# Performance work log

Hardware: AMD Instinct MI355X
Metric: run time of the kernel (lower is better)

## Reference

```python
import jax, jax.numpy as jnp
import numpy as np

B, N, K = 2, 1024, 16
D_MODEL, D_ELLIP, N_HEADS = 768, 128, 8
NF = D_MODEL // 6            # sinusoidal freqs per coordinate
MAX_LOG_FREQ = 7.0
ENC_H = max(1, N_HEADS // 2) # ellipsoid encoder heads
ENC_FF = 2048                # torch TransformerEncoderLayer default dim_feedforward


def setup_inputs() -> dict:
    key = jax.random.key(0)
    ks = jax.random.split(key, 20)
    rn = lambda k, sh, sc=1.0: jax.random.normal(k, sh, dtype=jnp.float32) * sc
    w = lambda k, o, i: rn(k, (o, i), 1.0 / np.sqrt(i))
    inp = {}
    inp['s'] = rn(ks[0], (B, N, D_MODEL))
    inp['R'] = rn(ks[1], (B, N, 3, 3))
    inp['t'] = rn(ks[2], (B, N, 3))
    inp['ellip_tokens'] = rn(ks[3], (B, K, D_ELLIP))
    inp['mu'] = rn(ks[4], (B, K, 3))
    inp['Sigma'] = rn(ks[5], (B, K, 3, 3))
    inp['ellip_mask'] = jnp.ones((B, K), dtype=jnp.bool_)
    # main attention params (torch Linear convention: [out, in])
    inp['mix_w'] = w(ks[6], 6 * NF, 6 * NF)
    inp['lin_cov_w'] = w(ks[7], D_MODEL, 9)
    inp['q_w'] = w(ks[8], D_MODEL, D_MODEL)
    inp['k_w'] = w(ks[9], D_MODEL, 2 * D_MODEL)
    inp['v_w'] = w(ks[10], D_MODEL, D_MODEL + D_ELLIP)
    inp['o_w'] = w(ks[11], D_MODEL, D_MODEL)
    # ellipsoid TransformerEncoderLayer params (post-norm, eval mode)
    inp['enc_in_w'] = w(ks[12], 3 * D_ELLIP, D_ELLIP)
    inp['enc_in_b'] = jnp.zeros((3 * D_ELLIP,), jnp.float32)
    inp['enc_out_w'] = w(ks[13], D_ELLIP, D_ELLIP)
    inp['enc_out_b'] = jnp.zeros((D_ELLIP,), jnp.float32)
    inp['lin1_w'] = w(ks[14], ENC_FF, D_ELLIP)
    inp['lin1_b'] = jnp.zeros((ENC_FF,), jnp.float32)
    inp['lin2_w'] = w(ks[15], D_ELLIP, ENC_FF)
    inp['lin2_b'] = jnp.zeros((D_ELLIP,), jnp.float32)
    inp['ln1_g'] = jnp.ones((D_ELLIP,), jnp.float32)
    inp['ln1_b'] = jnp.zeros((D_ELLIP,), jnp.float32)
    inp['ln2_g'] = jnp.ones((D_ELLIP,), jnp.float32)
    inp['ln2_b'] = jnp.zeros((D_ELLIP,), jnp.float32)
    return inp


def _layernorm(x, g, b, eps=1e-5):
    m = x.mean(-1, keepdims=True)
    v = ((x - m) ** 2).mean(-1, keepdims=True)
    return (x - m) / jnp.sqrt(v + eps) * g + b


def _fwd(s, R, t, ellip_tokens, mu, Sigma, mix_w, lin_cov_w, q_w, k_w, v_w, o_w,
         enc_in_w, enc_in_b, enc_out_w, enc_out_b, lin1_w, lin1_b, lin2_w, lin2_b,
         ln1_g, ln1_b, ln2_g, ln2_b, ellip_mask):
    # --- ellipsoid self-attn encoder (single post-norm layer, eval mode) ---
    x = ellip_tokens                                   # [B,K,de]
    qkv = x @ enc_in_w.T + enc_in_b
    q, kk, v = jnp.split(qkv, 3, axis=-1)
    dhe = D_ELLIP // ENC_H
    qh = q.reshape(B, K, ENC_H, dhe)
    kh = kk.reshape(B, K, ENC_H, dhe)
    vh = v.reshape(B, K, ENC_H, dhe)
    sc = jnp.einsum('bqhd,bkhd->bhqk', qh, kh) / np.sqrt(dhe).astype(np.float32)
    ao = jnp.einsum('bhqk,bkhd->bqhd', jax.nn.softmax(sc, -1), vh).reshape(B, K, D_ELLIP)
    ao = ao @ enc_out_w.T + enc_out_b
    x = _layernorm(x + ao, ln1_g, ln1_b)
    ff = jax.nn.relu(x @ lin1_w.T + lin1_b) @ lin2_w.T + lin2_b
    e = _layernorm(x + ff, ln2_g, ln2_b)               # [B,K,de]
    # --- per-query local frame transforms ---
    diff = mu[:, None, :, :] - t[:, :, None, :]        # [B,N,K,3]
    r = jnp.einsum('bnji,bnkj->bnki', R, diff)         # R^T @ diff
    C = jnp.einsum('bnji,bkjl,bnlm->bnkim', R, Sigma, R)  # R^T Sigma R [B,N,K,3,3]
    # --- sinusoidal posenc (sin first, then cos; flatten coord-major) ---
    freqs = 2.0 ** jnp.linspace(0.0, MAX_LOG_FREQ, NF).astype(jnp.float32)
    xf = r[..., None] * freqs                          # [B,N,K,3,NF]
    feat = jnp.concatenate([jnp.sin(xf), jnp.cos(xf)], axis=-2).reshape(B, N, K, 6 * NF)
    pos = feat @ mix_w.T                               # [B,N,K,d]
    cov = C.reshape(B, N, K, 9) @ lin_cov_w.T          # [B,N,K,d]
    K_mat = jnp.concatenate([pos, cov], -1) @ k_w.T    # [B,N,K,d]
    eB = jnp.broadcast_to(e[:, None, :, :], (B, N, K, D_ELLIP))
    V_mat = jnp.concatenate([pos, eB], -1) @ v_w.T     # [B,N,K,d]
    Q = s @ q_w.T                                      # [B,N,d]
    dh = D_MODEL // N_HEADS
    Qh = Q.reshape(B, N, N_HEADS, dh)
    Kh = K_mat.reshape(B, N, K, N_HEADS, dh)
    Vh = V_mat.reshape(B, N, K, N_HEADS, dh)
    scores = jnp.einsum('bnhd,bnkhd->bnhk', Qh, Kh) / np.sqrt(dh).astype(np.float32)
    scores = scores + (1.0 - ellip_mask.astype(scores.dtype))[:, None, None, :] * -10000.0
    attn = jax.nn.softmax(scores, -1)                  # [B,N,H,K]
    out = jnp.einsum('bnhk,bnkhd->bnhd', attn, Vh).reshape(B, N, D_MODEL)
    return out @ o_w.T


def reference(s, R, t, ellip_tokens, mu, Sigma, mix_w, lin_cov_w, q_w, k_w, v_w, o_w,
              enc_in_w, enc_in_b, enc_out_w, enc_out_b, lin1_w, lin1_b, lin2_w, lin2_b,
              ln1_g, ln1_b, ln2_g, ln2_b, ellip_mask):
    return _fwd(s, R, t, ellip_tokens, mu, Sigma, mix_w, lin_cov_w, q_w, k_w, v_w, o_w,
                enc_in_w, enc_in_b, enc_out_w, enc_out_b, lin1_w, lin1_b, lin2_w, lin2_b,
                ln1_g, ln1_b, ln2_g, ln2_b, ellip_mask)
```

## Files before the change

kernel.cpp:

```cpp
#include <hip/hip_runtime.h>
#include <math.h>

#define BB     2
#define SEQ    1024
#define KTOK   16
#define DM     768
#define DE     128
#define NH     8
#define DHD    96
#define EH     4
#define DHE    32
#define EFF    2048

typedef short short8 __attribute__((ext_vector_type(8)));
typedef float f32x4 __attribute__((ext_vector_type(4)));
typedef unsigned short ushort_t;

__device__ __forceinline__ void split2(float x, ushort_t& h, ushort_t& l) {
  unsigned u = __float_as_uint(x);
  unsigned hb = (u + 0x7fffu + ((u >> 16) & 1u)) >> 16;
  float hf = __uint_as_float(hb << 16);
  float r = x - hf;
  unsigned u2 = __float_as_uint(r);
  unsigned lb = (u2 + 0x7fffu + ((u2 >> 16) & 1u)) >> 16;
  h = (ushort_t)hb;
  l = (ushort_t)lb;
}

typedef const unsigned int __attribute__((address_space(1)))* gas_p;
typedef unsigned int __attribute__((address_space(3)))* las_p;
__device__ __forceinline__ void load_lds16(const ushort_t* g, ushort_t* l) {
  __builtin_amdgcn_global_load_lds((gas_p)g, (las_p)l, 16, 0, 0);
}

template<int OMODE, bool ADD>
__device__ __forceinline__ void gemm_body(
    ushort_t (*AhB)[2048], ushort_t (*AlB)[2048],
    ushort_t (*BhB)[2048], ushort_t (*BlB)[2048],
    const ushort_t* A, int lda, int aC0, int aLoOff,
    const ushort_t* B, int ldb, int bC0, int bLoOff,
    void* Cv, int ldc, int cLoOff,
    const float* av, int ldadd,
    int row0, int col0, int N, int K)
{
  int tid = threadIdx.x;
  int wave = tid >> 6, lane = tid & 63;
  int quad = lane >> 4, mrow = lane & 15;
  int wm = (wave >> 1) * 32, wn = (wave & 1) * 32;
  int sr = tid >> 2, q8 = (tid & 3) << 3;
  int wbase = wave << 9;
  f32x4 acc[2][2] = {};

  const ushort_t* pa = A + (long)(row0 + sr) * lda + (aC0 + q8);
  const ushort_t* pb = B + (long)(col0 + sr) * ldb + (bC0 + q8);

  load_lds16(pa, &AhB[0][wbase]);
  load_lds16(pa + aLoOff, &AlB[0][wbase]);
  load_lds16(pb, &BhB[0][wbase]);
  load_lds16(pb + bLoOff, &BlB[0][wbase]);

  int buf = 0;
  for (int k0 = 0; k0 < K; k0 += 32) {
    __syncthreads();
    if (k0 + 32 < K) {
      int kn = k0 + 32;
      load_lds16(pa + kn, &AhB[buf ^ 1][wbase]);
      load_lds16(pa + aLoOff + kn, &AlB[buf ^ 1][wbase]);
      load_lds16(pb + kn, &BhB[buf ^ 1][wbase]);
      load_lds16(pb + bLoOff + kn, &BlB[buf ^ 1][wbase]);
    }
    short8 fah[2], fal[2], fbh[2], fbl[2];
    #pragma unroll
    for (int t = 0; t < 2; t++) {
      fah[t] = *(const short8*)&AhB[buf][(wm + t * 16 + mrow) * 32 + (quad << 3)];
      fal[t] = *(const short8*)&AlB[buf][(wm + t * 16 + mrow) * 32 + (quad << 3)];
      fbh[t] = *(const short8*)&BhB[buf][(wn + t * 16 + mrow) * 32 + (quad << 3)];
      fbl[t] = *(const short8*)&BlB[buf][(wn + t * 16 + mrow) * 32 + (quad << 3)];
    }
    #pragma unroll
    for (int mt = 0; mt < 2; mt++)
      #pragma unroll
      for (int nt = 0; nt < 2; nt++) {
        f32x4 c = acc[mt][nt];
        c = __builtin_amdgcn_mfma_f32_16x16x32_bf16(fah[mt], fbh[nt], c, 0, 0, 0);
        c = __builtin_amdgcn_mfma_f32_16x16x32_bf16(fal[mt], fbh[nt], c, 0, 0, 0);
        c = __builtin_amdgcn_mfma_f32_16x16x32_bf16(fah[mt], fbl[nt], c, 0, 0, 0);
        acc[mt][nt] = c;
      }
    buf ^= 1;
  }
  float* Cf = (float*)Cv;
  ushort_t* Cs = (ushort_t*)Cv;
  #pragma unroll
  for (int mt = 0; mt < 2; mt++)
    #pragma unroll
    for (int nt = 0; nt < 2; nt++) {
      int col = col0 + wn + nt * 16 + mrow;
      if (col >= N) continue;
      int rb = row0 + wm + mt * 16 + (quad << 2);
      #pragma unroll
      for (int rr = 0; rr < 4; rr++) {
        float v = acc[mt][nt][rr];
        if (ADD) v += av[(long)(rb + rr) * ldadd + col];
        if (OMODE == 0) {
          Cf[(long)(rb + rr) * ldc + col] = v;
        } else {
          ushort_t h, l;
          split2(v, h, l);
          Cs[(long)(rb + rr) * ldc + col] = h;
          Cs[(long)(rb + rr) * ldc + cLoOff + col] = l;
        }
      }
    }
}

template<int OMODE, bool ADD>
__global__ __launch_bounds__(256) void gemm3t(
    const ushort_t* __restrict__ A, int lda, int aKstep, int aLoOff,
    const ushort_t* __restrict__ B, long bOffZ, int ldb, int bKstep, int bLoOff,
    void* __restrict__ Cv, int ldc, int cOffZ, int cLoOff,
    const float* __restrict__ addv, int ldadd, int addOffZ,
    int M, int N, int K)
{
  __shared__ ushort_t Ah[2][2048], Al[2][2048], Bh[2][2048], Bl[2][2048];
  int z = blockIdx.z;
  void* Cz = (OMODE == 0) ? (void*)((float*)Cv + (long)z * cOffZ)
                          : (void*)((ushort_t*)Cv + (long)z * cOffZ);
  gemm_body<OMODE, ADD>(Ah, Al, Bh, Bl,
      A, lda, z * aKstep, aLoOff,
      B + (long)z * bOffZ, ldb, z * bKstep, bLoOff,
      Cz, ldc, cLoOff,
      ADD ? addv + (long)z * addOffZ : nullptr, ldadd,
      blockIdx.y * 64, blockIdx.x * 64, N, K);
}

__global__ __launch_bounds__(256) void combo1(
    const float* __restrict__ s, const float* __restrict__ q_w,
    const float* __restrict__ o_w, const float* __restrict__ k_w,
    const float* __restrict__ v_w,
    ushort_t* __restrict__ sS, ushort_t* __restrict__ qwS,
    ushort_t* __restrict__ owS, ushort_t* __restrict__ kwS,
    ushort_t* __restrict__ vwS,
    const float* __restrict__ mix_w, ushort_t* __restrict__ mixTS,
    const float* __restrict__ tok, const float* __restrict__ enc_in_w,
    const float* __restrict__ enc_in_b, float* __restrict__ qkv,
    const float* __restrict__ lin_cov_w, float* __restrict__ Bk9)
{
  int r = blockIdx.x, tid = threadIdx.x;
  if (r < 3840) {
    const float* in; int ldin; ushort_t* out; int base;
    if (r < 1536)      { in = s;   ldin = DM;      out = sS;  base = 0; }
    else if (r < 2112) { in = q_w; ldin = DM;      out = qwS; base = 1536; }
    else if (r < 2688) { in = o_w; ldin = DM;      out = owS; base = 2112; }
    else if (r < 3264) { in = k_w; ldin = 2 * DM;  out = kwS; base = 2688; }
    else               { in = v_w; ldin = DM + DE; out = vwS; base = 3264; }
    long i = (long)(r - base) * 256 + tid;
    int rr = (int)(i / 192), c4 = (int)(i % 192) << 2;
    float4 v = *(const float4*)(in + (long)rr * ldin + c4);
    ushort_t h[4], l[4];
    split2(v.x, h[0], l[0]);
    split2(v.y, h[1], l[1]);
    split2(v.z, h[2], l[2]);
    split2(v.w, h[3], l[3]);
    ushort_t* orow = out + (long)rr * 1536;
    ushort4 hv; hv.x = h[0]; hv.y = h[1]; hv.z = h[2]; hv.w = h[3];
    ushort4 lv; lv.x = l[0]; lv.y = l[1]; lv.z = l[2]; lv.w = l[3];
    *(ushort4*)(orow + c4) = hv;
    *(ushort4*)(orow + DM + c4) = lv;
  } else if (r < 3984) {
    __shared__ float tile[64][65];
    int idx = r - 3840;
    int n0 = (idx % 12) * 64, k0 = (idx / 12) * 64;
    #pragma unroll
    for (int p = 0; p < 16; p++) {
      int q = p * 256 + tid;
      int rr = q >> 6, cc = q & 63;
      tile[rr][cc] = mix_w[(long)(k0 + rr) * DM + n0 + cc];
    }
    __syncthreads();
    #pragma unroll
    for (int p = 0; p < 16; p++) {
      int q = p * 256 + tid;
      int nr = q >> 6, kc = q & 63;
      ushort_t h, l;
      split2(tile[kc][nr], h, l);
      mixTS[(long)(n0 + nr) * 1536 + (k0 + kc)] = h;
      mixTS[(long)(n0 + nr) * 1536 + DM + (k0 + kc)] = l;
    }
  } else if (r < 4016) {
    __shared__ float xr[DE];
    int tkn = r - 3984;
    if (tid < DE) xr[tid] = tok[tkn * DE + tid];
    __syncthreads();
    for (int o = tid; o < 3 * DE; o += 256) {
      float acc = enc_in_b[o];
      const float4* wr = (const float4*)(enc_in_w + (long)o * DE);
      #pragma unroll 8
      for (int j = 0; j < DE / 4; j++) {
        float4 p = wr[j];
        acc = fmaf(p.x, xr[j * 4 + 0], acc);
        acc = fmaf(p.y, xr[j * 4 + 1], acc);
        acc = fmaf(p.z, xr[j * 4 + 2], acc);
        acc = fmaf(p.w, xr[j * 4 + 3], acc);
      }
      qkv[tkn * 384 + o] = acc;
    }
  } else {
    int idx = (r - 4016) * 256 + tid;
    if (idx < DM * 9) {
      int rr = idx / 9, p = idx % 9;
      const float* kr = k_w + (long)rr * (2 * DM) + DM;
      float acc = 0.f;
      for (int j = 0; j < DM; j++) acc = fmaf(kr[j], lin_cov_w[j * 9 + p], acc);
      Bk9[idx] = acc;
    }
  }
}

union MegaSmem {
  struct { ushort_t Ah[2][2048], Al[2][2048], Bh[2][2048], Bl[2][2048]; } g;
  struct {
    float qkvs[KTOK][384];
    float scl2[EH][KTOK], at2[EH][KTOK];
    float ao[DE], x1s[DE], el[DE];
    float ff1L[EFF];
    float part[256];
    float red[4], stats[2];
  } e;
};

__global__ __launch_bounds__(256) void mega1(
    const ushort_t* __restrict__ sS, const ushort_t* __restrict__ qwS,
    const ushort_t* __restrict__ mixTS, const ushort_t* __restrict__ kwS,
    const ushort_t* __restrict__ vwS,
    ushort_t* __restrict__ QS, ushort_t* __restrict__ AkTS,
    ushort_t* __restrict__ AvS,
    const float* __restrict__ tok, const float* __restrict__ qkvG,
    const float* __restrict__ out_w, const float* __restrict__ out_b,
    const float* __restrict__ ln1_g, const float* __restrict__ ln1_b,
    const float* __restrict__ lin1_w, const float* __restrict__ lin1_b,
    const float* __restrict__ lin2_w, const float* __restrict__ lin2_b,
    const float* __restrict__ ln2_g, const float* __restrict__ ln2_b,
    const float* __restrict__ v_w, float* __restrict__ evec)
{
  __shared__ MegaSmem sm;
  int blk = blockIdx.x, tid = threadIdx.x;
  if (blk < 672) {
    if (blk < 384) {
      gemm_body<1, false>(sm.g.Ah, sm.g.Al, sm.g.Bh, sm.g.Bl,
                          sS, 1536, 0, DM, qwS, 1536, 0, DM,
                          QS, 1536, DM, nullptr, 0,
                          (blk / 12) * 64, (blk % 12) * 64, DM, DM);
    } else if (blk < 528) {
      int t2 = blk - 384;
      gemm_body<1, false>(sm.g.Ah, sm.g.Al, sm.g.Bh, sm.g.Bl,
                          mixTS, 1536, 0, DM, kwS, 1536, 0, DM,
                          AkTS, 1536, DM, nullptr, 0,
                          (t2 / 12) * 64, (t2 % 12) * 64, DM, DM);
    } else {
      int t2 = blk - 528;
      gemm_body<1, false>(sm.g.Ah, sm.g.Al, sm.g.Bh, sm.g.Bl,
                          vwS, 1536, 0, DM, mixTS, 1536, 0, DM,
                          AvS, 1536, DM, nullptr, 0,
                          (t2 / 12) * 64, (t2 % 12) * 64, DM, DM);
    }
    return;
  }
  int idx = blk - 672;
  int b = idx >> 4, tk = idx & 15;
  for (int i = tid; i < KTOK * 384; i += 256)
    sm.e.qkvs[i / 384][i % 384] = qkvG[b * KTOK * 384 + i];
  __syncthreads();
  if (tid < EH * KTOK) {
    int h = tid >> 4, kk = tid & 15;
    float a = 0.f;
    #pragma unroll 8
    for (int d = 0; d < DHE; d++)
      a = fmaf(sm.e.qkvs[tk][h * DHE + d], sm.e.qkvs[kk][DE + h * DHE + d], a);
    sm.e.scl2[h][kk] = a * 0.17677669529663687f;
  }
  __syncthreads();
  if (tid < EH) {
    float m = -1e30f;
    for (int kk = 0; kk < KTOK; kk++) m = fmaxf(m, sm.e.scl2[tid][kk]);
    float smx = 0.f;
    for (int kk = 0; kk < KTOK; kk++) { float e = expf(sm.e.scl2[tid][kk] - m); sm.e.at2[tid][kk] = e; smx += e; }
    float inv = 1.f / smx;
    for (int kk = 0; kk < KTOK; kk++) sm.e.at2[tid][kk] *= inv;
  }
  __syncthreads();
  if (tid < DE) {
    int h = tid / DHE;
    float a = 0.f;
    #pragma unroll
    for (int kk = 0; kk < KTOK; kk++) a = fmaf(sm.e.at2[h][kk], sm.e.qkvs[kk][256 + tid], a);
    sm.e.ao[tid] = a;
  }
  __syncthreads();
  float val = 0.f;
  if (tid < DE) {
    float a = out_b[tid];
    const float4* wr = (const float4*)(out_w + (long)tid * DE);
    #pragma unroll 8
    for (int j = 0; j < DE / 4; j++) {
      float4 p = wr[j];
      a = fmaf(p.x, sm.e.ao[j * 4 + 0], a);
      a = fmaf(p.y, sm.e.ao[j * 4 + 1], a);
      a = fmaf(p.z, sm.e.ao[j * 4 + 2], a);
      a = fmaf(p.w, sm.e.ao[j * 4 + 3], a);
    }
    val = tok[idx * DE + tid] + a;
  }
  {
    float v = val;
    #pragma unroll
    for (int off = 32; off > 0; off >>= 1) v += __shfl_down(v, off);
    if ((tid & 63) == 0) sm.e.red[tid >> 6] = v;
    __syncthreads();
    if (tid == 0) sm.e.stats[0] = (sm.e.red[0] + sm.e.red[1] + sm.e.red[2] + sm.e.red[3]) * (1.f / DE);
    __syncthreads();
    float d = (tid < DE) ? (val - sm.e.stats[0]) : 0.f;
    float v2 = d * d;
    #pragma unroll
    for (int off = 32; off > 0; off >>= 1) v2 += __shfl_down(v2, off);
    if ((tid & 63) == 0) sm.e.red[tid >> 6] = v2;
    __syncthreads();
    if (tid == 0) sm.e.stats[1] = rsqrtf((sm.e.red[0] + sm.e.red[1] + sm.e.red[2] + sm.e.red[3]) * (1.f / DE) + 1e-5f);
    __syncthreads();
    if (tid < DE) sm.e.x1s[tid] = (val - sm.e.stats[0]) * sm.e.stats[1] * ln1_g[tid] + ln1_b[tid];
    __syncthreads();
  }
  for (int f = tid; f < EFF; f += 256) {
    float a = lin1_b[f];
    const float4* wr = (const float4*)(lin1_w + (long)f * DE);
    #pragma unroll 8
    for (int j = 0; j < DE / 4; j++) {
      float4 p = wr[j];
      a = fmaf(p.x, sm.e.x1s[j * 4 + 0], a);
      a = fmaf(p.y, sm.e.x1s[j * 4 + 1], a);
      a = fmaf(p.z, sm.e.x1s[j * 4 + 2], a);
      a = fmaf(p.w, sm.e.x1s[j * 4 + 3], a);
    }
    sm.e.ff1L[f] = fmaxf(a, 0.f);
  }
  __syncthreads();
  {
    int j = tid >> 1, half = tid & 1;
    const float4* wr = (const float4*)(lin2_w + (long)j * EFF + half * 1024);
    const float4* fr = (const float4*)(sm.e.ff1L + half * 1024);
    float a = 0.f;
    #pragma unroll 8
    for (int i = 0; i < 256; i++) {
      float4 p = wr[i], q = fr[i];
      a = fmaf(p.x, q.x, a);
      a = fmaf(p.y, q.y, a);
      a = fmaf(p.z, q.z, a);
      a = fmaf(p.w, q.w, a);
    }
    sm.e.part[tid] = a;
  }
  __syncthreads();
  float t2v = 0.f;
  if (tid < DE) t2v = sm.e.x1s[tid] + lin2_b[tid] + sm.e.part[2 * tid] + sm.e.part[2 * tid + 1];
  {
    float v = t2v;
    #pragma unroll
    for (int off = 32; off > 0; off >>= 1) v += __shfl_down(v, off);
    if ((tid & 63) == 0) sm.e.red[tid >> 6] = v;
    __syncthreads();
    if (tid == 0) sm.e.stats[0] = (sm.e.red[0] + sm.e.red[1] + sm.e.red[2] + sm.e.red[3]) * (1.f / DE);
    __syncthreads();
    float d = (tid < DE) ? (t2v - sm.e.stats[0]) : 0.f;
    float v2 = d * d;
    #pragma unroll
    for (int off = 32; off > 0; off >>= 1) v2 += __shfl_down(v2, off);
    if ((tid & 63) == 0) sm.e.red[tid >> 6] = v2;
    __syncthreads();
    if (tid == 0) sm.e.stats[1] = rsqrtf((sm.e.red[0] + sm.e.red[1] + sm.e.red[2] + sm.e.red[3]) * (1.f / DE) + 1e-5f);
    __syncthreads();
    if (tid < DE) sm.e.el[tid] = (t2v - sm.e.stats[0]) * sm.e.stats[1] * ln2_g[tid] + ln2_b[tid];
    __syncthreads();
  }
  #pragma unroll
  for (int q = 0; q < 3; q++) {
    int d = tid + (q << 8);
    float a = 0.f;
    const float4* wr = (const float4*)(v_w + (long)d * (DM + DE) + DM);
    #pragma unroll 8
    for (int j = 0; j < DE / 4; j++) {
      float4 p = wr[j];
      a = fmaf(p.x, sm.e.el[j * 4 + 0], a);
      a = fmaf(p.y, sm.e.el[j * 4 + 1], a);
      a = fmaf(p.z, sm.e.el[j * 4 + 2], a);
      a = fmaf(p.w, sm.e.el[j * 4 + 3], a);
    }
    evec[idx * DM + d] = a;
  }
}

__global__ __launch_bounds__(256) void qa_qb(
    const ushort_t* __restrict__ QS, const ushort_t* __restrict__ AkTS,
    float* __restrict__ QA, const float* __restrict__ Bk9,
    float* __restrict__ QB)
{
  __shared__ ushort_t Ah[2][2048], Al[2][2048], Bh[2][2048], Bl[2][2048];
  int r = blockIdx.x;
  if (r < 3072) {
    int z = r / 384, rr = r % 384;
    gemm_body<0, false>(Ah, Al, Bh, Bl,
        QS, 1536, z * DHD, DM, AkTS, 1536, z * DHD, DM,
        (void*)(QA + (long)z * DM), NH * DM, 0, nullptr, 0,
        (rr / 12) * 64, (rr % 12) * 64, DM, DHD);
  } else {
    int idx = (r - 3072) * 256 + threadIdx.x;
    if (idx < BB * SEQ * NH * 9) {
      int bn = idx / 72, rem = idx % 72, h = rem / 9, p = rem % 9;
      const ushort_t* qr = QS + (long)bn * 1536 + h * DHD;
      float acc = 0.f;
      for (int k = 0; k < DHD; k++) {
        float q = __uint_as_float((unsigned)qr[k] << 16) +
                  __uint_as_float((unsigned)qr[DM + k] << 16);
        acc = fmaf(q, Bk9[(h * DHD + k) * 9 + p], acc);
      }
      QB[idx] = acc;
    }
  }
}

__global__ __launch_bounds__(256) void main_attn(
    const float* __restrict__ Rg, const float* __restrict__ tg,
    const float* __restrict__ mug, const float* __restrict__ Sigg,
    const float* __restrict__ QAg, const float* __restrict__ QBg,
    const float* __restrict__ evec, ushort_t* __restrict__ wfeatS,
    float* __restrict__ outeG)
{
  int bn = blockIdx.x;
  int b = bn >> 10;
  int tid = threadIdx.x;
  int w = tid >> 6, lane = tid & 63;
  int h0 = 2 * w, h1 = 2 * w + 1;
  __shared__ float Rm[9], tm[3];
  __shared__ float rK[KTOK][3];
  __shared__ float C9[KTOK][9];
  __shared__ float featL[8][772];
  __shared__ float QBl[NH][12];
  __shared__ float scl[NH][KTOK];
  __shared__ float attnl[NH][KTOK];
  __shared__ float freqsL[128];
  float4 qa0[3], qa1[3];
  {
    const float* qbase = QAg + (long)bn * (NH * DM);
    #pragma unroll
    for (int g = 0; g < 3; g++) {
      qa0[g] = *(const float4*)&qbase[h0 * DM + g * 256 + (lane << 2)];
      qa1[g] = *(const float4*)&qbase[h1 * DM + g * 256 + (lane << 2)];
    }
  }
  if (tid < 9) Rm[tid] = Rg[bn * 9 + tid];
  if (tid >= 16 && tid < 19) tm[tid - 16] = tg[bn * 3 + (tid - 16)];
  if (tid >= 32 && tid < 32 + NH * 9) {
    int q = tid - 32;
    QBl[q / 9][q % 9] = QBg[bn * (NH * 9) + q];
  }
  if (tid >= 128) {
    const float step = 7.0f / 127.0f;
    freqsL[tid - 128] = exp2f(step * (float)(tid - 128));
  }
  __syncthreads();
  if (tid < KTOK) {
    int k = tid;
    float diff[3];
    #pragma unroll
    for (int j = 0; j < 3; j++) diff[j] = mug[(b * KTOK + k) * 3 + j] - tm[j];
    #pragma unroll
    for (int i = 0; i < 3; i++) {
      float a = 0.f;
      #pragma unroll
      for (int j = 0; j < 3; j++) a = fmaf(Rm[j * 3 + i], diff[j], a);
      rK[k][i] = a;
    }
    float SR[9];
    const float* Sg = Sigg + (b * KTOK + k) * 9;
    #pragma unroll
    for (int j = 0; j < 3; j++)
      #pragma unroll
      for (int m2 = 0; m2 < 3; m2++) {
        float a = 0.f;
        #pragma unroll
        for (int l = 0; l < 3; l++) a = fmaf(Sg[j * 3 + l], Rm[l * 3 + m2], a);
        SR[j * 3 + m2] = a;
      }
    #pragma unroll
    for (int i = 0; i < 3; i++)
      #pragma unroll
      for (int m2 = 0; m2 < 3; m2++) {
        float a = 0.f;
        #pragma unroll
        for (int j = 0; j < 3; j++) a = fmaf(Rm[j * 3 + i], SR[j * 3 + m2], a);
        C9[k][i * 3 + m2] = a;
      }
  }
  __syncthreads();
  for (int half = 0; half < 2; half++) {
    int kb = half * 8;
    for (int c = tid; c < 768; c += 256) {
      int k = c / 96, f0 = (c % 96) << 2;
      int coord = f0 >> 7;
      float rv = rK[kb + k][coord];
      float4 fr = *(const float4*)&freqsL[f0 & 127];
      float4 sv, cv;
      __sincosf(rv * fr.x, &sv.x, &cv.x);
      __sincosf(rv * fr.y, &sv.y, &cv.y);
      __sincosf(rv * fr.z, &sv.z, &cv.z);
      __sincosf(rv * fr.w, &sv.w, &cv.w);
      *(float4*)&featL[k][f0] = sv;
      *(float4*)&featL[k][384 + f0] = cv;
    }
    __syncthreads();
    for (int k = 0; k < 8; k++) {
      float a0 = 0.f, a1 = 0.f;
      #pragma unroll
      for (int g = 0; g < 3; g++) {
        float4 fv = *(const float4*)&featL[k][g * 256 + (lane << 2)];
        a0 = fmaf(qa0[g].x, fv.x, a0); a0 = fmaf(qa0[g].y, fv.y, a0);
        a0 = fmaf(qa0[g].z, fv.z, a0); a0 = fmaf(qa0[g].w, fv.w, a0);
        a1 = fmaf(qa1[g].x, fv.x, a1); a1 = fmaf(qa1[g].y, fv.y, a1);
        a1 = fmaf(qa1[g].z, fv.z, a1); a1 = fmaf(qa1[g].w, fv.w, a1);
      }
      #pragma unroll
      for (int off = 32; off > 0; off >>= 1) {
        a0 += __shfl_down(a0, off);
        a1 += __shfl_down(a1, off);
      }
      if (lane == 0) { scl[h0][kb + k] = a0; scl[h1][kb + k] = a1; }
    }
    __syncthreads();
  }
  if (tid < NH) {
    int h = tid;
    float vals[KTOK];
    float m = -1e30f;
    for (int k = 0; k < KTOK; k++) {
      float a = scl[h][k];
      #pragma unroll
      for (int p = 0; p < 9; p++) a = fmaf(C9[k][p], QBl[h][p], a);
      a *= 0.10206207261596575f;
      vals[k] = a;
      m = fmaxf(m, a);
    }
    float sm = 0.f;
    for (int k = 0; k < KTOK; k++) { float e = expf(vals[k] - m); attnl[h][k] = e; sm += e; }
    float inv = 1.f / sm;
    for (int k = 0; k < KTOK; k++) attnl[h][k] *= inv;
  }
  __syncthreads();
  float at0[KTOK], at1[KTOK];
  #pragma unroll
  for (int k = 0; k < KTOK; k++) { at0[k] = attnl[h0][k]; at1[k] = attnl[h1][k]; }
  float4 wf0[3] = {}, wf1[3] = {};
  for (int pass = 0; pass < 2; pass++) {
    int kb = (pass == 0) ? 8 : 0;
    if (pass == 1) {
      __syncthreads();
      for (int c = tid; c < 768; c += 256) {
        int k = c / 96, f0 = (c % 96) << 2;
        int coord = f0 >> 7;
        float rv = rK[k][coord];
        float4 fr = *(const float4*)&freqsL[f0 & 127];
        float4 sv, cv;
        __sincosf(rv * fr.x, &sv.x, &cv.x);
        __sincosf(rv * fr.y, &sv.y, &cv.y);
        __sincosf(rv * fr.z, &sv.z, &cv.z);
        __sincosf(rv * fr.w, &sv.w, &cv.w);
        *(float4*)&featL[k][f0] = sv;
        *(float4*)&featL[k][384 + f0] = cv;
      }
      __syncthreads();
    }
    #pragma unroll
    for (int g = 0; g < 3; g++) {
      float4 s0 = wf0[g], s1 = wf1[g];
      #pragma unroll
      for (int k = 0; k < 8; k++) {
        float4 fv = *(const float4*)&featL[k][g * 256 + (lane << 2)];
        float w0 = at0[kb + k], w1 = at1[kb + k];
        s0.x = fmaf(w0, fv.x, s0.x); s0.y = fmaf(w0, fv.y, s0.y);
        s0.z = fmaf(w0, fv.z, s0.z); s0.w = fmaf(w0, fv.w, s0.w);
        s1.x = fmaf(w1, fv.x, s1.x); s1.y = fmaf(w1, fv.y, s1.y);
        s1.z = fmaf(w1, fv.z, s1.z); s1.w = fmaf(w1, fv.w, s1.w);
      }
      wf0[g] = s0; wf1[g] = s1;
    }
  }
  {
    ushort_t* wrow = wfeatS + (long)bn * (2 * NH * DM);
    #pragma unroll
    for (int g = 0; g < 3; g++) {
      int jj = g * 256 + (lane << 2);
      ushort4 hv, lv;
      split2(wf0[g].x, hv.x, lv.x); split2(wf0[g].y, hv.y, lv.y);
      split2(wf0[g].z, hv.z, lv.z); split2(wf0[g].w, hv.w, lv.w);
      *(ushort4*)(wrow + h0 * DM + jj) = hv;
      *(ushort4*)(wrow + NH * DM + h0 * DM + jj) = lv;
      split2(wf1[g].x, hv.x, lv.x); split2(wf1[g].y, hv.y, lv.y);
      split2(wf1[g].z, hv.z, lv.z); split2(wf1[g].w, hv.w, lv.w);
      *(ushort4*)(wrow + h1 * DM + jj) = hv;
      *(ushort4*)(wrow + NH * DM + h1 * DM + jj) = lv;
    }
  }
  for (int d = tid; d < DM; d += 256) {
    int h = d / DHD;
    float acc = 0.f;
    #pragma unroll
    for (int k = 0; k < KTOK; k++)
      acc = fmaf(attnl[h][k], evec[(b * KTOK + k) * DM + d], acc);
    outeG[(long)bn * DM + d] = acc;
  }
}

extern "C" void kernel_launch(void* const* d_in, const int* in_sizes, int n_in,
                              void* d_out, int out_size, void* d_ws, size_t ws_size,
                              hipStream_t stream) {
  const float* s    = (const float*)d_in[0];
  const float* R    = (const float*)d_in[1];
  const float* t    = (const float*)d_in[2];
  const float* tok  = (const float*)d_in[3];
  const float* mu   = (const float*)d_in[4];
  const float* Sig  = (const float*)d_in[5];
  const float* mix_w     = (const float*)d_in[7];
  const float* lin_cov_w = (const float*)d_in[8];
  const float* q_w  = (const float*)d_in[9];
  const float* k_w  = (const float*)d_in[10];
  const float* v_w  = (const float*)d_in[11];
  const float* o_w  = (const float*)d_in[12];
  const float* enc_in_w  = (const float*)d_in[13];
  const float* enc_in_b  = (const float*)d_in[14];
  const float* enc_out_w = (const float*)d_in[15];
  const float* enc_out_b = (const float*)d_in[16];
  const float* lin1_w = (const float*)d_in[17];
  const float* lin1_b = (const float*)d_in[18];
  const float* lin2_w = (const float*)d_in[19];
  const float* lin2_b = (const float*)d_in[20];
  const float* ln1_g = (const float*)d_in[21];
  const float* ln1_b = (const float*)d_in[22];
  const float* ln2_g = (const float*)d_in[23];
  const float* ln2_b = (const float*)d_in[24];
  float* out = (float*)d_out;
  char* wsb  = (char*)d_ws;

  const int BN = BB * SEQ;
  float* qkv  = (float*)(wsb);
  float* evec = (float*)(wsb + 344064);
  float* Bk9  = (float*)(wsb + 442368);
  char* p = wsb + 470016;
  ushort_t* qwS   = (ushort_t*)p;  p += 2359296;
  ushort_t* owS   = (ushort_t*)p;  p += 2359296;
  ushort_t* kwS   = (ushort_t*)p;  p += 2359296;
  ushort_t* vwS   = (ushort_t*)p;  p += 2359296;
  ushort_t* mixTS = (ushort_t*)p;  p += 2359296;
  ushort_t* AkTS  = (ushort_t*)p;  p += 2359296;
  ushort_t* AvS   = (ushort_t*)p;  p += 2359296;
  ushort_t* sS    = (ushort_t*)p;  p += 6291456;
  ushort_t* QS    = (ushort_t*)p;  p += 6291456;
  float*    QB    = (float*)p;     p += 589824;
  float*    oute  = (float*)p;     p += 6291456;
  float*    QA    = (float*)p;     p += 50331648;
  ushort_t* wfeatS = (ushort_t*)QA;
  ushort_t* US     = sS;

  dim3 blk(256);

  combo1<<<4043, blk, 0, stream>>>(s, q_w, o_w, k_w, v_w,
                                   sS, qwS, owS, kwS, vwS,
                                   mix_w, mixTS,
                                   tok, enc_in_w, enc_in_b, qkv,
                                   lin_cov_w, Bk9);
  mega1<<<704, blk, 0, stream>>>(sS, qwS, mixTS, kwS, vwS, QS, AkTS, AvS,
                                 tok, qkv, enc_out_w, enc_out_b,
                                 ln1_g, ln1_b, lin1_w, lin1_b,
                                 lin2_w, lin2_b, ln2_g, ln2_b, v_w, evec);
  qa_qb<<<3648, blk, 0, stream>>>(QS, AkTS, QA, Bk9, QB);
  main_attn<<<BN, blk, 0, stream>>>(R, t, mu, Sig, QA, QB, evec, wfeatS, oute);
  gemm3t<1, true><<<dim3(2, 32, NH), blk, 0, stream>>>(
      wfeatS, 2 * NH * DM, DM, NH * DM,  AvS, (long)DHD * 1536, 1536, 0, DM,
      US, 1536, DHD, DM,  oute, DM, DHD,  BN, DHD, DM);
  gemm3t<0, false><<<dim3(12, 32, 1), blk, 0, stream>>>(
      US, 1536, 0, DM,  owS, 0, 1536, 0, DM,
      out, DM, 0, 0,  nullptr, 0, 0,  BN, DM, DM);
}
```

Measured before the change: 362.1 us.

## Split encoder FFN across blocks, defer attn·evec into GEMM epilogue, swizzle LDS

The per-token encoder FFN used to run serially in 32 tail blocks of mega1. It is now split into 8 slices per token inside qa_qb, with partial sums combined by atomicAdd, and the final LayerNorm plus v_w projection run in extra blocks of main_attn. main_attn no longer computes the attn·evec term. It writes the attention weights instead, and the new gemm_u kernel adds that term in its epilogue, so the oute buffer is no longer round-tripped through memory. The GEMM LDS reads and writes use an XOR swizzle to reduce bank conflicts. In exchange, float atomics make the accumulation order nondeterministic, and every GEMM tile's epilogue now reloads evec.

```diff
diff --git a/kernel.cpp b/kernel.cpp
--- a/kernel.cpp
+++ b/kernel.cpp
@@ -33,7 +33,7 @@
   __builtin_amdgcn_global_load_lds((gas_p)g, (las_p)l, 16, 0, 0);
 }
 
-template<int OMODE, bool ADD>
+template<int OMODE, int ADDMODE>
 __device__ __forceinline__ void gemm_body(
     ushort_t (*AhB)[2048], ushort_t (*AlB)[2048],
     ushort_t (*BhB)[2048], ushort_t (*BlB)[2048],
@@ -41,24 +41,27 @@
     const ushort_t* B, int ldb, int bC0, int bLoOff,
     void* Cv, int ldc, int cLoOff,
     const float* av, int ldadd,
+    const float* attnG, const float* evecG, int zhead,
     int row0, int col0, int N, int K)
 {
   int tid = threadIdx.x;
   int wave = tid >> 6, lane = tid & 63;
   int quad = lane >> 4, mrow = lane & 15;
   int wm = (wave >> 1) * 32, wn = (wave & 1) * 32;
-  int sr = tid >> 2, q8 = (tid & 3) << 3;
+  int sr = tid >> 2;
+  int qs = ((tid & 3) << 3) ^ (((sr >> 1) & 3) << 3);
   int wbase = wave << 9;
   f32x4 acc[2][2] = {};
 
-  const ushort_t* pa = A + (long)(row0 + sr) * lda + (aC0 + q8);
-  const ushort_t* pb = B + (long)(col0 + sr) * ldb + (bC0 + q8);
+  const ushort_t* pa = A + (long)(row0 + sr) * lda + (aC0 + qs);
+  const ushort_t* pb = B + (long)(col0 + sr) * ldb + (bC0 + qs);
 
   load_lds16(pa, &AhB[0][wbase]);
   load_lds16(pa + aLoOff, &AlB[0][wbase]);
   load_lds16(pb, &BhB[0][wbase]);
   load_lds16(pb + bLoOff, &BlB[0][wbase]);
 
+  int co = (quad << 3) ^ (((mrow >> 1) & 3) << 3);
   int buf = 0;
   for (int k0 = 0; k0 < K; k0 += 32) {
     __syncthreads();
@@ -72,10 +75,10 @@
     short8 fah[2], fal[2], fbh[2], fbl[2];
     #pragma unroll
     for (int t = 0; t < 2; t++) {
-      fah[t] = *(const short8*)&AhB[buf][(wm + t * 16 + mrow) * 32 + (quad << 3)];
-      fal[t] = *(const short8*)&AlB[buf][(wm + t * 16 + mrow) * 32 + (quad << 3)];
-      fbh[t] = *(const short8*)&BhB[buf][(wn + t * 16 + mrow) * 32 + (quad << 3)];
-      fbl[t] = *(const short8*)&BlB[buf][(wn + t * 16 + mrow) * 32 + (quad << 3)];
+      fah[t] = *(const short8*)&AhB[buf][(wm + t * 16 + mrow) * 32 + co];
+      fal[t] = *(const short8*)&AlB[buf][(wm + t * 16 + mrow) * 32 + co];
+      fbh[t] = *(const short8*)&BhB[buf][(wn + t * 16 + mrow) * 32 + co];
+      fbl[t] = *(const short8*)&BlB[buf][(wn + t * 16 + mrow) * 32 + co];
     }
     #pragma unroll
     for (int mt = 0; mt < 2; mt++)
@@ -91,6 +94,40 @@
   }
   float* Cf = (float*)Cv;
   ushort_t* Cs = (ushort_t*)Cv;
+  if (ADDMODE == 2) {
+    int b16 = (row0 >> 10) * 16;
+    float ev[2][16];
+    #pragma unroll
+    for (int nt = 0; nt < 2; nt++) {
+      int col = col0 + wn + nt * 16 + mrow;
+      int d = zhead * DHD + ((col < N) ? col : 0);
+      #pragma unroll
+      for (int k = 0; k < 16; k++) ev[nt][k] = evecG[(long)(b16 + k) * DM + d];
+    }
+    #pragma unroll
+    for (int mt = 0; mt < 2; mt++)
+      #pragma unroll
+      for (int rr = 0; rr < 4; rr++) {
+        int row = row0 + wm + mt * 16 + (quad << 2) + rr;
+        const float4* ar = (const float4*)(attnG + (long)row * 128 + zhead * 16);
+        float4 a0 = ar[0], a1 = ar[1], a2 = ar[2], a3 = ar[3];
+        float at[16] = {a0.x, a0.y, a0.z, a0.w, a1.x, a1.y, a1.z, a1.w,
+                        a2.x, a2.y, a2.z, a2.w, a3.x, a3.y, a3.z, a3.w};
+        #pragma unroll
+        for (int nt = 0; nt < 2; nt++) {
+          int col = col0 + wn + nt * 16 + mrow;
+          if (col >= N) continue;
+          float v = acc[mt][nt][rr];
+          #pragma unroll
+          for (int k = 0; k < 16; k++) v = fmaf(at[k], ev[nt][k], v);
+          ushort_t h, l;
+          split2(v, h, l);
+          Cs[(long)row * ldc + col] = h;
+          Cs[(long)row * ldc + cLoOff + col] = l;
+        }
+      }
+    return;
+  }
   #pragma unroll
   for (int mt = 0; mt < 2; mt++)
     #pragma unroll
@@ -101,7 +138,7 @@
       #pragma unroll
       for (int rr = 0; rr < 4; rr++) {
         float v = acc[mt][nt][rr];
-        if (ADD) v += av[(long)(rb + rr) * ldadd + col];
+        if (ADDMODE == 1) v += av[(long)(rb + rr) * ldadd + col];
         if (OMODE == 0) {
           Cf[(long)(rb + rr) * ldc + col] = v;
         } else {
@@ -112,26 +149,6 @@
         }
       }
     }
-}
-
-template<int OMODE, bool ADD>
-__global__ __launch_bounds__(256) void gemm3t(
-    const ushort_t* __restrict__ A, int lda, int aKstep, int aLoOff,
-    const ushort_t* __restrict__ B, long bOffZ, int ldb, int bKstep, int bLoOff,
-    void* __restrict__ Cv, int ldc, int cOffZ, int cLoOff,
-    const float* __restrict__ addv, int ldadd, int addOffZ,
-    int M, int N, int K)
-{
-  __shared__ ushort_t Ah[2][2048], Al[2][2048], Bh[2][2048], Bl[2][2048];
-  int z = blockIdx.z;
-  void* Cz = (OMODE == 0) ? (void*)((float*)Cv + (long)z * cOffZ)
-                          : (void*)((ushort_t*)Cv + (long)z * cOffZ);
-  gemm_body<OMODE, ADD>(Ah, Al, Bh, Bl,
-      A, lda, z * aKstep, aLoOff,
-      B + (long)z * bOffZ, ldb, z * bKstep, bLoOff,
-      Cz, ldc, cLoOff,
-      ADD ? addv + (long)z * addOffZ : nullptr, ldadd,
-      blockIdx.y * 64, blockIdx.x * 64, N, K);
 }
 
 __global__ __launch_bounds__(256) void combo1(
@@ -222,9 +239,7 @@
   struct {
     float qkvs[KTOK][384];
     float scl2[EH][KTOK], at2[EH][KTOK];
-    float ao[DE], x1s[DE], el[DE];
-    float ff1L[EFF];
-    float part[256];
+    float ao[DE];
     float red[4], stats[2];
   } e;
 };
@@ -238,31 +253,29 @@
     const float* __restrict__ tok, const float* __restrict__ qkvG,
     const float* __restrict__ out_w, const float* __restrict__ out_b,
     const float* __restrict__ ln1_g, const float* __restrict__ ln1_b,
-    const float* __restrict__ lin1_w, const float* __restrict__ lin1_b,
-    const float* __restrict__ lin2_w, const float* __restrict__ lin2_b,
-    const float* __restrict__ ln2_g, const float* __restrict__ ln2_b,
-    const float* __restrict__ v_w, float* __restrict__ evec)
+    const float* __restrict__ lin2_b,
+    float* __restrict__ x1G, float* __restrict__ tmp2G)
 {
   __shared__ MegaSmem sm;
   int blk = blockIdx.x, tid = threadIdx.x;
   if (blk < 672) {
     if (blk < 384) {
-      gemm_body<1, false>(sm.g.Ah, sm.g.Al, sm.g.Bh, sm.g.Bl,
-                          sS, 1536, 0, DM, qwS, 1536, 0, DM,
-                          QS, 1536, DM, nullptr, 0,
-                          (blk / 12) * 64, (blk % 12) * 64, DM, DM);
+      gemm_body<1, 0>(sm.g.Ah, sm.g.Al, sm.g.Bh, sm.g.Bl,
+                      sS, 1536, 0, DM, qwS, 1536, 0, DM,
+                      QS, 1536, DM, nullptr, 0, nullptr, nullptr, 0,
+                      (blk / 12) * 64, (blk % 12) * 64, DM, DM);
     } else if (blk < 528) {
       int t2 = blk - 384;
-      gemm_body<1, false>(sm.g.Ah, sm.g.Al, sm.g.Bh, sm.g.Bl,
-                          mixTS, 1536, 0, DM, kwS, 1536, 0, DM,
-                          AkTS, 1536, DM, nullptr, 0,
-                          (t2 / 12) * 64, (t2 % 12) * 64, DM, DM);
+      gemm_body<1, 0>(sm.g.Ah, sm.g.Al, sm.g.Bh, sm.g.Bl,
+                      mixTS, 1536, 0, DM, kwS, 1536, 0, DM,
+                      AkTS, 1536, DM, nullptr, 0, nullptr, nullptr, 0,
+                      (t2 / 12) * 64, (t2 % 12) * 64, DM, DM);
     } else {
       int t2 = blk - 528;
-      gemm_body<1, false>(sm.g.Ah, sm.g.Al, sm.g.Bh, sm.g.Bl,
-                          vwS, 1536, 0, DM, mixTS, 1536, 0, DM,
-                          AvS, 1536, DM, nullptr, 0,
-                          (t2 / 12) * 64, (t2 % 12) * 64, DM, DM);
+      gemm_body<1, 0>(sm.g.Ah, sm.g.Al, sm.g.Bh, sm.g.Bl,
+                      vwS, 1536, 0, DM, mixTS, 1536, 0, DM,
+                      AvS, 1536, DM, nullptr, 0, nullptr, nullptr, 0,
+                      (t2 / 12) * 64, (t2 % 12) * 64, DM, DM);
     }
     return;
   }
@@ -327,92 +340,32 @@
     __syncthreads();
     if (tid == 0) sm.e.stats[1] = rsqrtf((sm.e.red[0] + sm.e.red[1] + sm.e.red[2] + sm.e.red[3]) * (1.f / DE) + 1e-5f);
     __syncthreads();
-    if (tid < DE) sm.e.x1s[tid] = (val - sm.e.stats[0]) * sm.e.stats[1] * ln1_g[tid] + ln1_b[tid];
-    __syncthreads();
-  }
-  for (int f = tid; f < EFF; f += 256) {
-    float a = lin1_b[f];
-    const float4* wr = (const float4*)(lin1_w + (long)f * DE);
-    #pragma unroll 8
-    for (int j = 0; j < DE / 4; j++) {
-      float4 p = wr[j];
-      a = fmaf(p.x, sm.e.x1s[j * 4 + 0], a);
-      a = fmaf(p.y, sm.e.x1s[j * 4 + 1], a);
-      a = fmaf(p.z, sm.e.x1s[j * 4 + 2], a);
-      a = fmaf(p.w, sm.e.x1s[j * 4 + 3], a);
-    }
-    sm.e.ff1L[f] = fmaxf(a, 0.f);
-  }
-  __syncthreads();
-  {
-    int j = tid >> 1, half = tid & 1;
-    const float4* wr = (const float4*)(lin2_w + (long)j * EFF + half * 1024);
-    const float4* fr = (const float4*)(sm.e.ff1L + half * 1024);
-    float a = 0.f;
-    #pragma unroll 8
-    for (int i = 0; i < 256; i++) {
-      float4 p = wr[i], q = fr[i];
-      a = fmaf(p.x, q.x, a);
-      a = fmaf(p.y, q.y, a);
-      a = fmaf(p.z, q.z, a);
-      a = fmaf(p.w, q.w, a);
-    }
-    sm.e.part[tid] = a;
-  }
-  __syncthreads();
-  float t2v = 0.f;
-  if (tid < DE) t2v = sm.e.x1s[tid] + lin2_b[tid] + sm.e.part[2 * tid] + sm.e.part[2 * tid + 1];
-  {
-    float v = t2v;
-    #pragma unroll
-    for (int off = 32; off > 0; off >>= 1) v += __shfl_down(v, off);
-    if ((tid & 63) == 0) sm.e.red[tid >> 6] = v;
-    __syncthreads();
-    if (tid == 0) sm.e.stats[0] = (sm.e.red[0] + sm.e.red[1] + sm.e.red[2] + sm.e.red[3]) * (1.f / DE);
-    __syncthreads();
-    float d = (tid < DE) ? (t2v - sm.e.stats[0]) : 0.f;
-    float v2 = d * d;
-    #pragma unroll
-    for (int off = 32; off > 0; off >>= 1) v2 += __shfl_down(v2, off);
-    if ((tid & 63) == 0) sm.e.red[tid >> 6] = v2;
-    __syncthreads();
-    if (tid == 0) sm.e.stats[1] = rsqrtf((sm.e.red[0] + sm.e.red[1] + sm.e.red[2] + sm.e.red[3]) * (1.f / DE) + 1e-5f);
-    __syncthreads();
-    if (tid < DE) sm.e.el[tid] = (t2v - sm.e.stats[0]) * sm.e.stats[1] * ln2_g[tid] + ln2_b[tid];
-    __syncthreads();
-  }
-  #pragma unroll
-  for (int q = 0; q < 3; q++) {
-    int d = tid + (q << 8);
-    float a = 0.f;
-    const float4* wr = (const float4*)(v_w + (long)d * (DM + DE) + DM);
-    #pragma unroll 8
-    for (int j = 0; j < DE / 4; j++) {
-      float4 p = wr[j];
-      a = fmaf(p.x, sm.e.el[j * 4 + 0], a);
-      a = fmaf(p.y, sm.e.el[j * 4 + 1], a);
-      a = fmaf(p.z, sm.e.el[j * 4 + 2], a);
-      a = fmaf(p.w, sm.e.el[j * 4 + 3], a);
-    }
-    evec[idx * DM + d] = a;
+    if (tid < DE) {
+      float xn = (val - sm.e.stats[0]) * sm.e.stats[1] * ln1_g[tid] + ln1_b[tid];
+      x1G[idx * DE + tid] = xn;
+      tmp2G[idx * DE + tid] = xn + lin2_b[tid];
+    }
   }
 }
 
 __global__ __launch_bounds__(256) void qa_qb(
     const ushort_t* __restrict__ QS, const ushort_t* __restrict__ AkTS,
     float* __restrict__ QA, const float* __restrict__ Bk9,
-    float* __restrict__ QB)
+    float* __restrict__ QB,
+    const float* __restrict__ x1G, const float* __restrict__ lin1_w,
+    const float* __restrict__ lin1_b, const float* __restrict__ lin2_w,
+    float* __restrict__ tmp2G)
 {
   __shared__ ushort_t Ah[2][2048], Al[2][2048], Bh[2][2048], Bl[2][2048];
-  int r = blockIdx.x;
+  int r = blockIdx.x, tid = threadIdx.x;
   if (r < 3072) {
     int z = r / 384, rr = r % 384;
-    gemm_body<0, false>(Ah, Al, Bh, Bl,
+    gemm_body<0, 0>(Ah, Al, Bh, Bl,
         QS, 1536, z * DHD, DM, AkTS, 1536, z * DHD, DM,
-        (void*)(QA + (long)z * DM), NH * DM, 0, nullptr, 0,
+        (void*)(QA + (long)z * DM), NH * DM, 0, nullptr, 0, nullptr, nullptr, 0,
         (rr / 12) * 64, (rr % 12) * 64, DM, DHD);
-  } else {
-    int idx = (r - 3072) * 256 + threadIdx.x;
+  } else if (r < 3648) {
+    int idx = (r - 3072) * 256 + tid;
     if (idx < BB * SEQ * NH * 9) {
       int bn = idx / 72, rem = idx % 72, h = rem / 9, p = rem % 9;
       const ushort_t* qr = QS + (long)bn * 1536 + h * DHD;
@@ -424,6 +377,46 @@
       }
       QB[idx] = acc;
     }
+  } else {
+    __shared__ float x1s[DE];
+    __shared__ float ff1s[256];
+    __shared__ float part[256];
+    int idx2 = r - 3648;
+    int t = idx2 >> 3, slice = idx2 & 7;
+    if (tid < DE) x1s[tid] = x1G[t * DE + tid];
+    __syncthreads();
+    {
+      int f = slice * 256 + tid;
+      float a = lin1_b[f];
+      const float4* wr = (const float4*)(lin1_w + (long)f * DE);
+      #pragma unroll 8
+      for (int j = 0; j < DE / 4; j++) {
+        float4 p = wr[j];
+        a = fmaf(p.x, x1s[j * 4 + 0], a);
+        a = fmaf(p.y, x1s[j * 4 + 1], a);
+        a = fmaf(p.z, x1s[j * 4 + 2], a);
+        a = fmaf(p.w, x1s[j * 4 + 3], a);
+      }
+      ff1s[tid] = fmaxf(a, 0.f);
+    }
+    __syncthreads();
+    {
+      int j = tid & 127, fh = tid >> 7;
+      const float4* wr = (const float4*)(lin2_w + (long)j * EFF + slice * 256 + fh * 128);
+      const float4* fr = (const float4*)(ff1s + fh * 128);
+      float a = 0.f;
+      #pragma unroll 8
+      for (int i = 0; i < 32; i++) {
+        float4 p = wr[i], q = fr[i];
+        a = fmaf(p.x, q.x, a);
+        a = fmaf(p.y, q.y, a);
+        a = fmaf(p.z, q.z, a);
+        a = fmaf(p.w, q.w, a);
+      }
+      part[tid] = a;
+    }
+    __syncthreads();
+    if (tid < DE) atomicAdd(&tmp2G[t * DE + tid], part[tid] + part[tid + 128]);
   }
 }
 
@@ -431,12 +424,56 @@
     const float* __restrict__ Rg, const float* __restrict__ tg,
     const float* __restrict__ mug, const float* __restrict__ Sigg,
     const float* __restrict__ QAg, const float* __restrict__ QBg,
-    const float* __restrict__ evec, ushort_t* __restrict__ wfeatS,
-    float* __restrict__ outeG)
+    ushort_t* __restrict__ wfeatS, float* __restrict__ attnG,
+    const float* __restrict__ tmp2G, const float* __restrict__ ln2_g,
+    const float* __restrict__ ln2_b, const float* __restrict__ v_w,
+    float* __restrict__ evec)
 {
   int bn = blockIdx.x;
+  int tid = threadIdx.x;
+  if (bn >= BB * SEQ) {
+    __shared__ float el[DE];
+    __shared__ float red2[4];
+    __shared__ float stats2[2];
+    int idx = bn - BB * SEQ;
+    float val = (tid < DE) ? tmp2G[idx * DE + tid] : 0.f;
+    {
+      float v = val;
+      #pragma unroll
+      for (int off = 32; off > 0; off >>= 1) v += __shfl_down(v, off);
+      if ((tid & 63) == 0) red2[tid >> 6] = v;
+      __syncthreads();
+      if (tid == 0) stats2[0] = (red2[0] + red2[1] + red2[2] + red2[3]) * (1.f / DE);
+      __syncthreads();
+      float d = (tid < DE) ? (val - stats2[0]) : 0.f;
+      float v2 = d * d;
+      #pragma unroll
+      for (int off = 32; off > 0; off >>= 1) v2 += __shfl_down(v2, off);
+      if ((tid & 63) == 0) red2[tid >> 6] = v2;
+      __syncthreads();
+      if (tid == 0) stats2[1] = rsqrtf((red2[0] + red2[1] + red2[2] + red2[3]) * (1.f / DE) + 1e-5f);
+      __syncthreads();
+      if (tid < DE) el[tid] = (val - stats2[0]) * stats2[1] * ln2_g[tid] + ln2_b[tid];
+      __syncthreads();
+    }
+    #pragma unroll
+    for (int q = 0; q < 3; q++) {
+      int d = tid + (q << 8);
+      float a = 0.f;
+      const float4* wr = (const float4*)(v_w + (long)d * (DM + DE) + DM);
+      #pragma unroll 8
+      for (int j = 0; j < DE / 4; j++) {
+        float4 p = wr[j];
+        a = fmaf(p.x, el[j * 4 + 0], a);
+        a = fmaf(p.y, el[j * 4 + 1], a);
+        a = fmaf(p.z, el[j * 4 + 2], a);
+        a = fmaf(p.w, el[j * 4 + 3], a);
+      }
+      evec[idx * DM + d] = a;
+    }
+    return;
+  }
   int b = bn >> 10;
-  int tid = threadIdx.x;
   int w = tid >> 6, lane = tid & 63;
   int h0 = 2 * w, h1 = 2 * w + 1;
   __shared__ float Rm[9], tm[3];
@@ -554,6 +591,7 @@
     for (int k = 0; k < KTOK; k++) attnl[h][k] *= inv;
   }
   __syncthreads();
+  if (tid < NH * KTOK) attnG[bn * 128 + tid] = attnl[tid >> 4][tid & 15];
   float at0[KTOK], at1[KTOK];
   #pragma unroll
   for (int k = 0; k < KTOK; k++) { at0[k] = attnl[h0][k]; at1[k] = attnl[h1][k]; }
@@ -608,14 +646,32 @@
       *(ushort4*)(wrow + NH * DM + h1 * DM + jj) = lv;
     }
   }
-  for (int d = tid; d < DM; d += 256) {
-    int h = d / DHD;
-    float acc = 0.f;
-    #pragma unroll
-    for (int k = 0; k < KTOK; k++)
-      acc = fmaf(attnl[h][k], evec[(b * KTOK + k) * DM + d], acc);
-    outeG[(long)bn * DM + d] = acc;
-  }
+}
+
+__global__ __launch_bounds__(256) void gemm_u(
+    const ushort_t* __restrict__ wfeatS, const ushort_t* __restrict__ AvS,
+    ushort_t* __restrict__ US, const float* __restrict__ attnG,
+    const float* __restrict__ evec)
+{
+  __shared__ ushort_t Ah[2][2048], Al[2][2048], Bh[2][2048], Bl[2][2048];
+  int z = blockIdx.z;
+  gemm_body<1, 2>(Ah, Al, Bh, Bl,
+      wfeatS, 2 * NH * DM, z * DM, NH * DM,
+      AvS + (long)z * DHD * 1536, 1536, 0, DM,
+      (void*)(US + z * DHD), 1536, DM,
+      nullptr, 0, attnG, evec, z,
+      blockIdx.y * 64, blockIdx.x * 64, DHD, DM);
+}
+
+__global__ __launch_bounds__(256) void gemm_out(
+    const ushort_t* __restrict__ US, const ushort_t* __restrict__ owS,
+    float* __restrict__ out)
+{
+  __shared__ ushort_t Ah[2][2048], Al[2][2048], Bh[2][2048], Bl[2][2048];
+  gemm_body<0, 0>(Ah, Al, Bh, Bl,
+      US, 1536, 0, DM, owS, 1536, 0, DM,
+      (void*)out, DM, 0, nullptr, 0, nullptr, nullptr, 0,
+      blockIdx.y * 64, blockIdx.x * 64, DM, DM);
 }
 
 extern "C" void kernel_launch(void* const* d_in, const int* in_sizes, int n_in,
@@ -650,6 +706,8 @@
 
   const int BN = BB * SEQ;
   float* qkv  = (float*)(wsb);
+  float* x1e  = (float*)(wsb + 49152);
+  float* t2e  = (float*)(wsb + 327680);
   float* evec = (float*)(wsb + 344064);
   float* Bk9  = (float*)(wsb + 442368);
   char* p = wsb + 470016;
@@ -663,7 +721,7 @@
   ushort_t* sS    = (ushort_t*)p;  p += 6291456;
   ushort_t* QS    = (ushort_t*)p;  p += 6291456;
   float*    QB    = (float*)p;     p += 589824;
-  float*    oute  = (float*)p;     p += 6291456;
+  float*    attnG = (float*)p;     p += 6291456;
   float*    QA    = (float*)p;     p += 50331648;
   ushort_t* wfeatS = (ushort_t*)QA;
   ushort_t* US     = sS;
@@ -677,14 +735,12 @@
                                    lin_cov_w, Bk9);
   mega1<<<704, blk, 0, stream>>>(sS, qwS, mixTS, kwS, vwS, QS, AkTS, AvS,
                                  tok, qkv, enc_out_w, enc_out_b,
-                                 ln1_g, ln1_b, lin1_w, lin1_b,
-                                 lin2_w, lin2_b, ln2_g, ln2_b, v_w, evec);
-  qa_qb<<<3648, blk, 0, stream>>>(QS, AkTS, QA, Bk9, QB);
-  main_attn<<<BN, blk, 0, stream>>>(R, t, mu, Sig, QA, QB, evec, wfeatS, oute);
-  gemm3t<1, true><<<dim3(2, 32, NH), blk, 0, stream>>>(
-      wfeatS, 2 * NH * DM, DM, NH * DM,  AvS, (long)DHD * 1536, 1536, 0, DM,
-      US, 1536, DHD, DM,  oute, DM, DHD,  BN, DHD, DM);
-  gemm3t<0, false><<<dim3(12, 32, 1), blk, 0, stream>>>(
-      US, 1536, 0, DM,  owS, 0, 1536, 0, DM,
-      out, DM, 0, 0,  nullptr, 0, 0,  BN, DM, DM);
-}
+                                 ln1_g, ln1_b, lin2_b, x1e, t2e);
+  qa_qb<<<3904, blk, 0, stream>>>(QS, AkTS, QA, Bk9, QB,
+                                  x1e, lin1_w, lin1_b, lin2_w, t2e);
+  main_attn<<<BN + 32, blk, 0, stream>>>(R, t, mu, Sig, QA, QB,
+                                         wfeatS, attnG,
+                                         t2e, ln2_g, ln2_b, v_w, evec);
+  gemm_u<<<dim3(2, 32, NH), blk, 0, stream>>>(wfeatS, AvS, US, attnG, evec);
+  gemm_out<<<dim3(12, 32, 1), blk, 0, stream>>>(US, owS, out);
+}
```

Result: faster. 315.2 us (-12.9%).
